# Kernel tuning notes

Hardware: AMD Instinct MI355X
Metric: run time of the kernel (lower is better)

Reference implementation:

```python
import jax, jax.numpy as jnp
import numpy as np

N = 50000


def gcn_conv(x, edge_index, W, b):
    # x: [N, F_in], edge_index: [2, E] (row=source j, col=target i)
    n = x.shape[0]
    loops = jnp.arange(n, dtype=edge_index.dtype)
    row = jnp.concatenate([edge_index[0], loops])
    col = jnp.concatenate([edge_index[1], loops])
    # linear transform first (PyG GCNConv)
    xw = x @ W  # [N, F_out]
    # symmetric normalization deg^{-1/2}[row] * deg^{-1/2}[col]
    deg = jax.ops.segment_sum(jnp.ones_like(col, dtype=xw.dtype), col, num_segments=n)
    dis = jnp.where(deg > 0, jax.lax.rsqrt(jnp.maximum(deg, 1e-12)), 0.0)
    norm = dis[row] * dis[col]  # [E+N]
    # gather-scale-scatter: sum_j norm_ij * (W x_j)
    msgs = xw[row] * norm[:, None]
    out = jax.ops.segment_sum(msgs, col, num_segments=n)
    return out + b


def setup_inputs() -> dict:
    key = jax.random.key(0)
    k1, k2, k3, k4, k5 = jax.random.split(key, 5)
    in_dim, hidden_dim, out_dim = 128, 128, 64
    x = jax.random.normal(k1, (N, in_dim), dtype=jnp.float32)
    edge_index = jax.random.randint(k2, (2, 800000), 0, N, dtype=jnp.int64)
    s1 = 1.0 / np.sqrt(in_dim)
    s2 = 1.0 / np.sqrt(hidden_dim)
    W1 = jax.random.uniform(k3, (in_dim, hidden_dim), jnp.float32, -s1, s1)
    b1 = jnp.zeros((hidden_dim,), jnp.float32)
    W2 = jax.random.uniform(k4, (hidden_dim, out_dim), jnp.float32, -s2, s2)
    b2 = jnp.zeros((out_dim,), jnp.float32)
    return {"x": x, "edge_index": edge_index, "W1": W1, "b1": b1, "W2": W2, "b2": b2}


def reference(x, edge_index, W1, b1, W2, b2):
    h = gcn_conv(x, edge_index, W1, b1)
    h = jax.nn.relu(h)
    # dropout(p=0.5, training=False) -> identity (inference reference)
    out = gcn_conv(h, edge_index, W2, b2)
    return out
```

## Files before the change

kernel.cpp:

```cpp
#include <hip/hip_runtime.h>
#include <hip/hip_fp16.h>


typedef _Float16 half8 __attribute__((ext_vector_type(8)));
typedef float floatx4 __attribute__((ext_vector_type(4)));

__global__ void k_count(const int* __restrict__ col, int* __restrict__ deg,
                        int* __restrict__ rank, int E) {
    int e = blockIdx.x * blockDim.x + threadIdx.x;
    if (e < E) rank[e] = atomicAdd(&deg[col[e]], 1);
}

__global__ __launch_bounds__(1024) void k_scan_local(const int* __restrict__ deg,
                                                     int* __restrict__ rowptr,
                                                     int* __restrict__ praw,
                                                     int* __restrict__ bsum,
                                                     float* __restrict__ dis, int n) {
    __shared__ int wsum[16];
    int b = blockIdx.x, tid = threadIdx.x;
    int lane = tid & 63, w = tid >> 6;
    int i = b * 1024 + tid;
    int v = (i < n) ? deg[i] : 0;
    if (i < n) dis[i] = rsqrtf((float)v + 1.0f);
    int sc = v;
#pragma unroll
    for (int off = 1; off < 64; off <<= 1) {
        int t = __shfl_up(sc, off);
        if (lane >= off) sc += t;
    }
    if (lane == 63) wsum[w] = sc;
    __syncthreads();
    if (w == 0) {
        int s = (lane < 16) ? wsum[lane] : 0;
#pragma unroll
        for (int off = 1; off < 16; off <<= 1) {
            int t = __shfl_up(s, off);
            if (lane >= off) s += t;
        }
        if (lane < 16) wsum[lane] = s;
    }
    __syncthreads();
    int incl = sc + ((w > 0) ? wsum[w - 1] : 0);
    if (i < n) {
        rowptr[i + 1] = incl;
        praw[i + 1] = incl;
    }
    if (tid == 1023) bsum[b] = incl;
    if (b == 0 && tid == 0) {
        rowptr[0] = 0;
        praw[0] = 0;
    }
}

template <int N, typename AT>
__device__ __forceinline__ void gemm_tile(const AT* __restrict__ X,
                                          const float* __restrict__ W,
                                          const float* __restrict__ scale,
                                          __half* __restrict__ Y, int M,
                                          int m0, __half2* wt, int tid) {
    for (int i = tid; i < N * 64; i += 256) {
        int nn = i & (N - 1);
        int k2 = i / N;
        float w0 = W[(size_t)(2 * k2) * N + nn];
        float w1 = W[(size_t)(2 * k2 + 1) * N + nn];
        wt[nn * 64 + ((k2 >> 2) ^ (nn & 15)) * 4 + (k2 & 3)] = __floats2half2_rn(w0, w1);
    }
    __syncthreads();
    int wid = tid >> 6, lane = tid & 63;
    int col = lane & 15, quad = lane >> 4;
    int m_a = m0 + wid * 16 + col;
    bool a_ok = m_a < M;
    constexpr int NT = N / 16;
    floatx4 acc[NT] = {};
#pragma unroll
    for (int ks = 0; ks < 4; ++ks) {
        int k = ks * 32 + quad * 8;
        half8 af;
        if constexpr (sizeof(AT) == 4) {
            floatx4 a0 = {0.f, 0.f, 0.f, 0.f}, a1 = {0.f, 0.f, 0.f, 0.f};
            if (a_ok) {
                a0 = *(const floatx4*)&X[(size_t)m_a * 128 + k];
                a1 = *(const floatx4*)&X[(size_t)m_a * 128 + k + 4];
            }
            af = half8{(_Float16)a0[0], (_Float16)a0[1], (_Float16)a0[2], (_Float16)a0[3],
                       (_Float16)a1[0], (_Float16)a1[1], (_Float16)a1[2], (_Float16)a1[3]};
        } else {
            half8 t = {};
            if (a_ok) t = *(const half8*)(const void*)&X[(size_t)m_a * 128 + k];
            af = t;
        }
        int kblk = ks * 4 + quad;
#pragma unroll
        for (int nt = 0; nt < NT; ++nt) {
            int nn = nt * 16 + col;
            half8 bf = *(const half8*)(const void*)&wt[nn * 64 + (kblk ^ (nn & 15)) * 4];
            acc[nt] = __builtin_amdgcn_mfma_f32_16x16x32_f16(af, bf, acc[nt], 0, 0, 0);
        }
    }
    int mbase = m0 + wid * 16 + quad * 4;
    float s[4];
#pragma unroll
    for (int r = 0; r < 4; ++r) s[r] = (mbase + r < M) ? scale[mbase + r] : 0.f;
#pragma unroll
    for (int nt = 0; nt < NT; ++nt) {
#pragma unroll
        for (int r = 0; r < 4; ++r) {
            if (mbase + r < M)
                Y[(size_t)(mbase + r) * N + nt * 16 + col] = __float2half(acc[nt][r] * s[r]);
        }
    }
}

__global__ __launch_bounds__(256) void k_fused(int* __restrict__ rowptr,
                                               const int* __restrict__ bsum, int n,
                                               const float* __restrict__ X,
                                               const float* __restrict__ W,
                                               const float* __restrict__ scale,
                                               __half* __restrict__ Y, int M,
                                               int FB, int GB,
                                               const int* __restrict__ praw,
                                               const int* __restrict__ row,
                                               const int* __restrict__ col,
                                               const int* __restrict__ rank,
                                               int* __restrict__ csr, int E) {
    __shared__ __align__(16) __half2 wt[128 * 64];
    int b = blockIdx.x, tid = threadIdx.x;
    if (b < FB) {
        int* red = (int*)wt;
        int partial = 0;
        for (int j = tid; j < b; j += 256) partial += bsum[j];
        red[tid] = partial;
        __syncthreads();
        for (int off = 128; off > 0; off >>= 1) {
            if (tid < off) red[tid] += red[tid + off];
            __syncthreads();
        }
        int offv = red[0];
        if (offv == 0) return;
#pragma unroll
        for (int r = 0; r < 4; ++r) {
            int i = b * 1024 + r * 256 + tid;
            if (i < n) rowptr[i + 1] += offv;
        }
        return;
    }
    if (b >= FB + GB) {
        int* q = (int*)wt;
        int nb = (n + 1023) >> 10;
        if (tid < 64) {
            int v = (tid >= 1 && tid <= nb) ? bsum[tid - 1] : 0;
#pragma unroll
            for (int off = 1; off < 64; off <<= 1) {
                int t = __shfl_up(v, off);
                if ((tid & 63) >= off) v += t;
            }
            q[tid] = v;
        }
        __syncthreads();
        int base = (b - FB - GB) * 1024;
#pragma unroll
        for (int r = 0; r < 4; ++r) {
            int e = base + r * 256 + tid;
            if (e < E) {
                int c = col[e];
                int qi = (c == 0) ? 0 : ((c - 1) >> 10);
                csr[praw[c] + q[qi] + rank[e]] = row[e];
            }
        }
        return;
    }
    gemm_tile<128, float>(X, W, scale, Y, M, (b - FB) * 64, wt, tid);
}

__global__ __launch_bounds__(256) void k_gemm2(const __half* __restrict__ X,
                                               const float* __restrict__ W,
                                               const float* __restrict__ scale,
                                               __half* __restrict__ Y, int M) {
    __shared__ __align__(16) __half2 wt[64 * 64];
    gemm_tile<64, __half>(X, W, scale, Y, M, blockIdx.x * 64, wt, threadIdx.x);
}

__global__ __launch_bounds__(256) void k_agg128(const __half* __restrict__ xw,
                                                const float* __restrict__ dis,
                                                const int* __restrict__ rowptr,
                                                const int* __restrict__ csr,
                                                const float* __restrict__ bias,
                                                __half* __restrict__ out, int n) {
    int tid = threadIdx.x;
    int lane = tid & 63;
    int q = lane >> 4, li = lane & 15;
    int qbase = lane & 48;
    int node = blockIdx.x * 16 + ((tid >> 6) << 2) + q;
    bool ok = node < n;
    float di = 0.f;
    int beg = 0, end = 0;
    if (ok) {
        di = dis[node];
        beg = rowptr[node];
        end = rowptr[node + 1];
    }
    int dg = end - beg;
    int m1 = max(dg, __shfl(dg, lane ^ 16));
    int mx = max(m1, __shfl(m1, lane ^ 32));
    const half8* rows = (const half8*)xw;
    float acc[8] = {};
    if (ok) {
        half8 sf = rows[(size_t)node * 16 + li];
#pragma unroll
        for (int f = 0; f < 8; ++f) acc[f] = (float)sf[f];
    }
    for (int i = 0; i < mx; i += 8) {
        int e = beg + i + (li & 7);
        int myidx = (e < end) ? csr[e] : 0;
        half8 v[8];
#pragma unroll
        for (int j = 0; j < 8; ++j) {
            int s = __shfl(myidx, qbase + j);
            v[j] = rows[(size_t)s * 16 + li];
        }
#pragma unroll
        for (int j = 0; j < 8; ++j) {
            if (beg + i + j < end) {
#pragma unroll
                for (int f = 0; f < 8; ++f) acc[f] += (float)v[j][f];
            }
        }
    }
    if (ok) {
        floatx4 b0 = *(const floatx4*)&bias[li * 8];
        floatx4 b1 = *(const floatx4*)&bias[li * 8 + 4];
        half8 o;
#pragma unroll
        for (int f = 0; f < 4; ++f) o[f] = (_Float16)fmaxf(acc[f] * di + b0[f], 0.f);
#pragma unroll
        for (int f = 0; f < 4; ++f) o[4 + f] = (_Float16)fmaxf(acc[4 + f] * di + b1[f], 0.f);
        ((half8*)out)[(size_t)node * 16 + li] = o;
    }
}

__global__ __launch_bounds__(256) void k_agg64(const __half* __restrict__ xw,
                                               const float* __restrict__ dis,
                                               const int* __restrict__ rowptr,
                                               const int* __restrict__ csr,
                                               const float* __restrict__ bias,
                                               float* __restrict__ out, int n) {
    int tid = threadIdx.x;
    int lane = tid & 63;
    int o8 = lane >> 3, li = lane & 7;
    int obase = lane & 56;
    int node = blockIdx.x * 32 + ((tid >> 6) << 3) + o8;
    bool ok = node < n;
    float di = 0.f;
    int beg = 0, end = 0;
    if (ok) {
        di = dis[node];
        beg = rowptr[node];
        end = rowptr[node + 1];
    }
    int dg = end - beg;
    int m1 = max(dg, __shfl(dg, lane ^ 8));
    int m2 = max(m1, __shfl(m1, lane ^ 16));
    int mx = max(m2, __shfl(m2, lane ^ 32));
    const half8* rows = (const half8*)xw;
    float acc[8] = {};
    if (ok) {
        half8 sf = rows[(size_t)node * 8 + li];
#pragma unroll
        for (int f = 0; f < 8; ++f) acc[f] = (float)sf[f];
    }
    for (int i = 0; i < mx; i += 8) {
        int e = beg + i + li;
        int myidx = (e < end) ? csr[e] : 0;
        half8 v[8];
#pragma unroll
        for (int j = 0; j < 8; ++j) {
            int s = __shfl(myidx, obase + j);
            v[j] = rows[(size_t)s * 8 + li];
        }
#pragma unroll
        for (int j = 0; j < 8; ++j) {
            if (beg + i + j < end) {
#pragma unroll
                for (int f = 0; f < 8; ++f) acc[f] += (float)v[j][f];
            }
        }
    }
    if (ok) {
        floatx4 b0 = *(const floatx4*)&bias[li * 8];
        floatx4 b1 = *(const floatx4*)&bias[li * 8 + 4];
        floatx4 o0, o1;
#pragma unroll
        for (int f = 0; f < 4; ++f) o0[f] = acc[f] * di + b0[f];
#pragma unroll
        for (int f = 0; f < 4; ++f) o1[f] = acc[4 + f] * di + b1[f];
        *(floatx4*)&out[(size_t)node * 64 + li * 8] = o0;
        *(floatx4*)&out[(size_t)node * 64 + li * 8 + 4] = o1;
    }
}

extern "C" void kernel_launch(void* const* d_in, const int* in_sizes, int n_in,
                              void* d_out, int out_size, void* d_ws, size_t ws_size,
                              hipStream_t stream) {
    const float* x  = (const float*)d_in[0];
    const int*   ei = (const int*)d_in[1];
    const float* W1 = (const float*)d_in[2];
    const float* b1 = (const float*)d_in[3];
    const float* W2 = (const float*)d_in[4];
    const float* b2 = (const float*)d_in[5];
    float* out = (float*)d_out;

    const int n = in_sizes[0] / 128;
    const int E = in_sizes[1] / 2;
    const int* row = ei;
    const int* col = ei + E;
    const int NB = (n + 1023) / 1024;
    const int CB = (E + 255) / 256;
    const int GB = (n + 63) / 64;
    const int FILLB = (E + 1023) / 1024;

    char* ws = (char*)d_ws;
    size_t off = 0;
    auto alloc = [&](size_t bytes) -> void* {
        void* p = ws + off;
        off += (bytes + 255) & ~(size_t)255;
        return p;
    };
    int*    deg    = (int*)alloc((size_t)n * 4);
    int*    rowptr = (int*)alloc((size_t)(n + 1) * 4);
    int*    praw   = (int*)alloc((size_t)(n + 1) * 4);
    int*    bsum   = (int*)alloc((size_t)NB * 4);
    int*    rank   = (int*)alloc((size_t)E * 4);
    int*    csr    = (int*)alloc((size_t)E * 4);
    float*  dis    = (float*)alloc((size_t)n * 4);
    __half* xw1    = (__half*)alloc((size_t)n * 128 * 2);
    __half* h      = (__half*)alloc((size_t)n * 128 * 2);
    __half* xw2    = (__half*)alloc((size_t)n * 64 * 2);
    (void)ws_size;

    hipMemsetAsync(deg, 0, (size_t)n * 4, stream);
    k_count<<<CB, 256, 0, stream>>>(col, deg, rank, E);
    k_scan_local<<<NB, 1024, 0, stream>>>(deg, rowptr, praw, bsum, dis, n);
    k_fused<<<NB + GB + FILLB, 256, 0, stream>>>(rowptr, bsum, n, x, W1, dis, xw1,
                                                 n, NB, GB, praw, row, col, rank,
                                                 csr, E);
    k_agg128<<<(n + 15) / 16, 256, 0, stream>>>(xw1, dis, rowptr, csr, b1, h, n);
    k_gemm2<<<GB, 256, 0, stream>>>(h, W2, dis, xw2, n);
    k_agg64<<<(n + 31) / 32, 256, 0, stream>>>(xw2, dis, rowptr, csr, b2, out, n);
}
```

Before: 201.8 us.

## Fuse layer-1 aggregation with layer-2 GEMM via shared-memory tile

Replaces the separate layer-1 aggregation kernel and the layer-2 GEMM with one kernel. Each block aggregates 64 nodes into a shared-memory fp16 tile (with bias and ReLU), then multiplies the tile by W2 using MFMA and writes the scaled result. This removes the intermediate hidden buffer's global write and read and one launch. In exchange it uses fewer, larger blocks with more shared memory, which may reduce latency hiding in the gather phase.

```diff
diff --git a/kernel.cpp b/kernel.cpp
--- a/kernel.cpp
+++ b/kernel.cpp
@@ -172,69 +172,107 @@
     gemm_tile<128, float>(X, W, scale, Y, M, (b - FB) * 64, wt, tid);
 }
 
-__global__ __launch_bounds__(256) void k_gemm2(const __half* __restrict__ X,
-                                               const float* __restrict__ W,
-                                               const float* __restrict__ scale,
-                                               __half* __restrict__ Y, int M) {
+__global__ __launch_bounds__(256) void k_agg_gemm(const __half* __restrict__ xw,
+                                                  const float* __restrict__ dis,
+                                                  const int* __restrict__ rowptr,
+                                                  const int* __restrict__ csr,
+                                                  const float* __restrict__ bias,
+                                                  const float* __restrict__ W2,
+                                                  __half* __restrict__ Y,
+                                                  int n) {
+    __shared__ __align__(16) half8 htile[64 * 16];
     __shared__ __align__(16) __half2 wt[64 * 64];
-    gemm_tile<64, __half>(X, W, scale, Y, M, blockIdx.x * 64, wt, threadIdx.x);
-}
-
-__global__ __launch_bounds__(256) void k_agg128(const __half* __restrict__ xw,
-                                                const float* __restrict__ dis,
-                                                const int* __restrict__ rowptr,
-                                                const int* __restrict__ csr,
-                                                const float* __restrict__ bias,
-                                                __half* __restrict__ out, int n) {
-    int tid = threadIdx.x;
-    int lane = tid & 63;
+    int tid = threadIdx.x, b = blockIdx.x;
+    int lane = tid & 63, w = tid >> 6;
     int q = lane >> 4, li = lane & 15;
     int qbase = lane & 48;
-    int node = blockIdx.x * 16 + ((tid >> 6) << 2) + q;
-    bool ok = node < n;
-    float di = 0.f;
-    int beg = 0, end = 0;
-    if (ok) {
-        di = dis[node];
-        beg = rowptr[node];
-        end = rowptr[node + 1];
-    }
-    int dg = end - beg;
-    int m1 = max(dg, __shfl(dg, lane ^ 16));
-    int mx = max(m1, __shfl(m1, lane ^ 32));
+
+    for (int i = tid; i < 64 * 64; i += 256) {
+        int nn = i & 63;
+        int k2 = i >> 6;
+        float w0 = W2[(size_t)(2 * k2) * 64 + nn];
+        float w1 = W2[(size_t)(2 * k2 + 1) * 64 + nn];
+        wt[nn * 64 + ((k2 >> 2) ^ (nn & 15)) * 4 + (k2 & 3)] = __floats2half2_rn(w0, w1);
+    }
+
     const half8* rows = (const half8*)xw;
-    float acc[8] = {};
-    if (ok) {
-        half8 sf = rows[(size_t)node * 16 + li];
-#pragma unroll
-        for (int f = 0; f < 8; ++f) acc[f] = (float)sf[f];
-    }
-    for (int i = 0; i < mx; i += 8) {
-        int e = beg + i + (li & 7);
-        int myidx = (e < end) ? csr[e] : 0;
-        half8 v[8];
-#pragma unroll
-        for (int j = 0; j < 8; ++j) {
-            int s = __shfl(myidx, qbase + j);
-            v[j] = rows[(size_t)s * 16 + li];
-        }
-#pragma unroll
-        for (int j = 0; j < 8; ++j) {
-            if (beg + i + j < end) {
-#pragma unroll
-                for (int f = 0; f < 8; ++f) acc[f] += (float)v[j][f];
-            }
-        }
-    }
-    if (ok) {
-        floatx4 b0 = *(const floatx4*)&bias[li * 8];
-        floatx4 b1 = *(const floatx4*)&bias[li * 8 + 4];
-        half8 o;
-#pragma unroll
-        for (int f = 0; f < 4; ++f) o[f] = (_Float16)fmaxf(acc[f] * di + b0[f], 0.f);
-#pragma unroll
-        for (int f = 0; f < 4; ++f) o[4 + f] = (_Float16)fmaxf(acc[4 + f] * di + b1[f], 0.f);
-        ((half8*)out)[(size_t)node * 16 + li] = o;
+    floatx4 bb0 = *(const floatx4*)&bias[li * 8];
+    floatx4 bb1 = *(const floatx4*)&bias[li * 8 + 4];
+
+#pragma unroll
+    for (int g = 0; g < 4; ++g) {
+        int m_loc = g * 16 + (w << 2) + q;
+        int node = b * 64 + m_loc;
+        bool ok = node < n;
+        float di = 0.f;
+        int beg = 0, end = 0;
+        if (ok) {
+            di = dis[node];
+            beg = rowptr[node];
+            end = rowptr[node + 1];
+        }
+        int dg = end - beg;
+        int m1 = max(dg, __shfl(dg, lane ^ 16));
+        int mx = max(m1, __shfl(m1, lane ^ 32));
+        float acc[8] = {};
+        if (ok) {
+            half8 sf = rows[(size_t)node * 16 + li];
+#pragma unroll
+            for (int f = 0; f < 8; ++f) acc[f] = (float)sf[f];
+        }
+        for (int i = 0; i < mx; i += 8) {
+            int e = beg + i + (li & 7);
+            int myidx = (e < end) ? csr[e] : 0;
+            half8 v[8];
+#pragma unroll
+            for (int j = 0; j < 8; ++j) {
+                int s = __shfl(myidx, qbase + j);
+                v[j] = rows[(size_t)s * 16 + li];
+            }
+#pragma unroll
+            for (int j = 0; j < 8; ++j) {
+                if (beg + i + j < end) {
+#pragma unroll
+                    for (int f = 0; f < 8; ++f) acc[f] += (float)v[j][f];
+                }
+            }
+        }
+        half8 o = {};
+        if (ok) {
+#pragma unroll
+            for (int f = 0; f < 4; ++f) o[f] = (_Float16)fmaxf(acc[f] * di + bb0[f], 0.f);
+#pragma unroll
+            for (int f = 0; f < 4; ++f) o[4 + f] = (_Float16)fmaxf(acc[4 + f] * di + bb1[f], 0.f);
+        }
+        htile[m_loc * 16 + (li ^ (m_loc & 7))] = o;
+    }
+    __syncthreads();
+
+    int col16 = lane & 15, quad = lane >> 4;
+    int m_loc = w * 16 + col16;
+    floatx4 gacc[4] = {};
+#pragma unroll
+    for (int ks = 0; ks < 4; ++ks) {
+        half8 af = htile[m_loc * 16 + ((ks * 4 + quad) ^ (m_loc & 7))];
+        int kblk = ks * 4 + quad;
+#pragma unroll
+        for (int nt = 0; nt < 4; ++nt) {
+            int nn = nt * 16 + col16;
+            half8 bf = *(const half8*)(const void*)&wt[nn * 64 + (kblk ^ (nn & 15)) * 4];
+            gacc[nt] = __builtin_amdgcn_mfma_f32_16x16x32_f16(af, bf, gacc[nt], 0, 0, 0);
+        }
+    }
+    int mbase = b * 64 + w * 16 + quad * 4;
+    float s[4];
+#pragma unroll
+    for (int r = 0; r < 4; ++r) s[r] = (mbase + r < n) ? dis[mbase + r] : 0.f;
+#pragma unroll
+    for (int nt = 0; nt < 4; ++nt) {
+#pragma unroll
+        for (int r = 0; r < 4; ++r) {
+            if (mbase + r < n)
+                Y[(size_t)(mbase + r) * 64 + nt * 16 + col16] = __float2half(gacc[nt][r] * s[r]);
+        }
     }
 }
 
@@ -333,7 +371,6 @@
     int*    csr    = (int*)alloc((size_t)E * 4);
     float*  dis    = (float*)alloc((size_t)n * 4);
     __half* xw1    = (__half*)alloc((size_t)n * 128 * 2);
-    __half* h      = (__half*)alloc((size_t)n * 128 * 2);
     __half* xw2    = (__half*)alloc((size_t)n * 64 * 2);
     (void)ws_size;
 
@@ -343,7 +380,6 @@
     k_fused<<<NB + GB + FILLB, 256, 0, stream>>>(rowptr, bsum, n, x, W1, dis, xw1,
                                                  n, NB, GB, praw, row, col, rank,
                                                  csr, E);
-    k_agg128<<<(n + 15) / 16, 256, 0, stream>>>(xw1, dis, rowptr, csr, b1, h, n);
-    k_gemm2<<<GB, 256, 0, stream>>>(h, W2, dis, xw2, n);
+    k_agg_gemm<<<GB, 256, 0, stream>>>(xw1, dis, rowptr, csr, b1, W2, xw2, n);
     k_agg64<<<(n + 31) / 32, 256, 0, stream>>>(xw2, dis, rowptr, csr, b2, out, n);
 }
```

New measurement: 198.8 us. About the same (-1.5%).
